# Kernel optimization log

Hardware: AMD Instinct MI355X
Metric: run time of the kernel (lower is better)

## Reference

```python
import jax, jax.numpy as jnp
import numpy as np

T, B, I, H = 512, 256, 256, 256


def setup_inputs() -> dict:
    key = jax.random.key(0)
    ks = jax.random.split(key, 4)
    s = 1.0 / np.sqrt(I + H)  # fan-in scaling like nn.Linear default
    return {
        "x": jax.random.normal(ks[0], (T, B, I), dtype=jnp.float32),
        "h": jnp.zeros((B, H), dtype=jnp.float32),
        "Wz_w": jax.random.normal(ks[1], (H, I + H), dtype=jnp.float32) * s,
        "Wz_b": jnp.zeros((H,), dtype=jnp.float32),
        "Wr_w": jax.random.normal(ks[2], (H, I + H), dtype=jnp.float32) * s,
        "Wr_b": jnp.zeros((H,), dtype=jnp.float32),
        "W_w": jax.random.normal(ks[3], (H, I + H), dtype=jnp.float32) * s,
        "W_b": jnp.zeros((H,), dtype=jnp.float32),
    }


def reference(x, h, Wz_w, Wz_b, Wr_w, Wr_b, W_w, W_b):
    # x: [T, B, I], h: [B, H]. Gate input order is cat(h, x) as in the torch code.
    def step(h, xt):
        gate = jnp.concatenate([h, xt], axis=1)              # [B, H+I]
        zt = jax.nn.sigmoid(gate @ Wz_w.T + Wz_b)            # [B, H]
        rt = jax.nn.sigmoid(gate @ Wr_w.T + Wr_b)            # [B, H]
        cand_in = jnp.concatenate([rt * h, xt], axis=1)      # [B, H+I]
        ht = (1.0 - zt) * h + zt * jnp.tanh(cand_in @ W_w.T + W_b)
        return ht, ht

    h_final, hAll = jax.lax.scan(step, h, x)                 # hAll: [T, B, H]
    return hAll, h_final
```

## Files before the change

### kernel.cpp

```cpp
#include <hip/hip_runtime.h>


typedef float f32x4 __attribute__((ext_vector_type(4)));
typedef short bf16x8 __attribute__((ext_vector_type(8)));

__device__ __forceinline__ unsigned short f2bf(float f) {
  union { float f; unsigned int u; } v; v.f = f;
  unsigned int u = v.u + 0x7fffu + ((v.u >> 16) & 1u);
  return (unsigned short)(u >> 16);
}
__device__ __forceinline__ float u2f(unsigned int u) {
  union { unsigned int u; float f; } v; v.u = u; return v.f;
}
__device__ __forceinline__ unsigned int cvt_pk_bf16(float lo, float hi) {
  unsigned int r;
  asm("v_cvt_pk_bf16_f32 %0, %1, %2" : "=v"(r) : "v"(lo), "v"(hi));
  return r;
}
__device__ __forceinline__ float sigmoid_f(float x) {
  return __builtin_amdgcn_rcpf(1.f + __expf(-x));
}
__device__ __forceinline__ float tanh_f(float x) {
  float e = __expf(2.f * x);
  return 1.f - 2.f * __builtin_amdgcn_rcpf(e + 1.f);
}
__device__ __forceinline__ f32x4 unpk(uint2 gv) {
  f32x4 a;
  a[0] = u2f(gv.x << 16); a[1] = u2f(gv.x & 0xffff0000u);
  a[2] = u2f(gv.y << 16); a[3] = u2f(gv.y & 0xffff0000u);
  return a;
}
__device__ __forceinline__ int frag_off(int j, int b) {
  return ((j >> 5) * 64 + ((j >> 3) & 3) * 16 + b) * 8 + (j & 7);
}

__global__ __launch_bounds__(256) void gru_gx_kernel(
    const float* __restrict__ x,
    const float* __restrict__ Wz, const float* __restrict__ Wr, const float* __restrict__ Wc,
    const float* __restrict__ bz, const float* __restrict__ br, const float* __restrict__ bc,
    unsigned short* __restrict__ gx)
{
  __shared__ __align__(16) unsigned short As[64][72];
  __shared__ __align__(16) unsigned short Bs[64][72];

  const int tid  = threadIdx.x;
  const int lane = tid & 63;
  const int wid  = tid >> 6;
  const int l15  = lane & 15;
  const int lg   = lane >> 4;
  const int m0   = blockIdx.x * 64;
  const int by   = blockIdx.y;
  const int gate = by >> 2;
  const int jb   = (by & 3) * 64;
  const float* W    = (gate == 0) ? Wz : ((gate == 1) ? Wr : Wc);
  const float* bias = (gate == 0) ? bz : ((gate == 1) ? br : bc);

  f32x4 acc[4];
  #pragma unroll
  for (int n = 0; n < 4; ++n) acc[n] = (f32x4){0.f, 0.f, 0.f, 0.f};

  for (int k0 = 0; k0 < 256; k0 += 64) {
    #pragma unroll
    for (int i = 0; i < 4; ++i) {
      int idx = tid + i * 256;
      int row = idx >> 4;
      int kq  = (idx & 15) << 2;
      float4 va = *(const float4*)(x + (size_t)(m0 + row) * 256 + k0 + kq);
      ushort4 ua; ua.x = f2bf(va.x); ua.y = f2bf(va.y); ua.z = f2bf(va.z); ua.w = f2bf(va.w);
      *(ushort4*)&As[row][kq] = ua;
      float4 vb = *(const float4*)(W + (size_t)(jb + row) * 512 + 256 + k0 + kq);
      ushort4 ub; ub.x = f2bf(vb.x); ub.y = f2bf(vb.y); ub.z = f2bf(vb.z); ub.w = f2bf(vb.w);
      *(ushort4*)&Bs[row][kq] = ub;
    }
    __syncthreads();
    #pragma unroll
    for (int ks = 0; ks < 64; ks += 32) {
      bf16x8 af = *(const bf16x8*)&As[wid * 16 + l15][ks + lg * 8];
      #pragma unroll
      for (int n = 0; n < 4; ++n) {
        bf16x8 bf = *(const bf16x8*)&Bs[n * 16 + l15][ks + lg * 8];
        acc[n] = __builtin_amdgcn_mfma_f32_16x16x32_bf16(af, bf, acc[n], 0, 0, 0);
      }
    }
    __syncthreads();
  }

  #pragma unroll
  for (int n = 0; n < 4; ++n) {
    float bv = bias[jb + n * 16 + l15];
    #pragma unroll
    for (int r = 0; r < 4; ++r) {
      As[wid * 16 + lg * 4 + r][n * 16 + l15] = f2bf(acc[n][r] + bv);
    }
  }
  __syncthreads();

  const int tt    = m0 >> 8;
  const int b0    = m0 & 255;
  const int jbase = by * 64;
  #pragma unroll
  for (int i = 0; i < 2; ++i) {
    int u    = tid + i * 256;
    int bg_l = u >> 7;
    int rem  = u & 127;
    int cb_l = rem >> 3;
    int bp   = rem & 7;
    int row0 = bg_l * 16 + bp * 2;
    uint2 lo = *(const uint2*)&As[row0][cb_l * 4];
    uint2 hi = *(const uint2*)&As[row0 + 1][cb_l * 4];
    uint4 val; val.x = lo.x; val.y = lo.y; val.z = hi.x; val.w = hi.y;
    size_t off = (((size_t)tt * 16 + (b0 >> 4) + bg_l) * 192 + (jbase >> 2) + cb_l) * 64
                 + (size_t)bp * 8;
    *(uint4*)(gx + off) = val;
  }
}

__global__ __launch_bounds__(512, 1) void gru_rec_kernel(
    const unsigned short* __restrict__ gx,
    const float* __restrict__ h0,
    const float* __restrict__ Wz, const float* __restrict__ Wr, const float* __restrict__ Wc,
    float* __restrict__ out)
{
  __shared__ __align__(16) unsigned short hA[4096];
  __shared__ __align__(16) unsigned short rhA[4096];

  const int tid   = threadIdx.x;
  const int lane  = tid & 63;
  const int wid   = tid >> 6;
  const int l15   = lane & 15;
  const int lg    = lane >> 4;
  const int wg    = blockIdx.x;
  const int brow0 = wg * 16;
  const int cb    = wid * 32;

  bf16x8 wz[2][8], wr[2][8], wc[2][8];
  #pragma unroll
  for (int n = 0; n < 2; ++n) {
    const int j = cb + n * 16 + l15;
    #pragma unroll
    for (int kk = 0; kk < 8; ++kk) {
      const int k = kk * 32 + lg * 8;
      #pragma unroll
      for (int g = 0; g < 3; ++g) {
        const float* W = (g == 0) ? Wz : ((g == 1) ? Wr : Wc);
        const float* p = W + (size_t)j * 512 + k;
        float4 a = *(const float4*)p;
        float4 b = *(const float4*)(p + 4);
        bf16x8 f;
        f[0] = (short)f2bf(a.x); f[1] = (short)f2bf(a.y);
        f[2] = (short)f2bf(a.z); f[3] = (short)f2bf(a.w);
        f[4] = (short)f2bf(b.x); f[5] = (short)f2bf(b.y);
        f[6] = (short)f2bf(b.z); f[7] = (short)f2bf(b.w);
        if (g == 0) wz[n][kk] = f; else if (g == 1) wr[n][kk] = f; else wc[n][kk] = f;
      }
    }
  }

  f32x4 hreg[2];
  #pragma unroll
  for (int n = 0; n < 2; ++n)
    hreg[n] = *(const f32x4*)(h0 + (size_t)(brow0 + l15) * 256 + cb + n * 16 + lg * 4);
  for (int idx = tid; idx < 16 * 256; idx += 512) {
    int r = idx >> 8, c = idx & 255;
    hA[frag_off(c, r)] = f2bf(h0[(size_t)(brow0 + r) * 256 + c]);
  }

  uint2 g1z[2], g1r[2], g2[2];
  {
    const size_t tb = (size_t)wg * 12288;
    #pragma unroll
    for (int n = 0; n < 2; ++n) {
      g1z[n] = *(const uint2*)(gx + tb + (size_t)(wid * 8 + n * 4 + lg) * 64 + l15 * 4);
      g1r[n] = *(const uint2*)(gx + tb + (size_t)(64 + wid * 8 + n * 4 + lg) * 64 + l15 * 4);
      g2[n]  = *(const uint2*)(gx + tb + (size_t)(128 + wid * 8 + n * 4 + lg) * 64 + l15 * 4);
    }
  }
  __syncthreads();

  for (int t = 0; t < 512; ++t) {
    const int tn = (t < 511) ? (t + 1) : 511;
    const size_t tbn = ((size_t)tn * 16 + wg) * 12288;

    f32x4 accZ[2], accR[2];
    #pragma unroll
    for (int n = 0; n < 2; ++n) { accZ[n] = unpk(g1z[n]); accR[n] = unpk(g1r[n]); }
    #pragma unroll
    for (int n = 0; n < 2; ++n) {
      g1z[n] = *(const uint2*)(gx + tbn + (size_t)(wid * 8 + n * 4 + lg) * 64 + l15 * 4);
      g1r[n] = *(const uint2*)(gx + tbn + (size_t)(64 + wid * 8 + n * 4 + lg) * 64 + l15 * 4);
    }

    #pragma unroll
    for (int kk = 0; kk < 8; ++kk) {
      bf16x8 hf = *(const bf16x8*)&hA[kk * 512 + lane * 8];
      accZ[0] = __builtin_amdgcn_mfma_f32_16x16x32_bf16(wz[0][kk], hf, accZ[0], 0, 0, 0);
      accZ[1] = __builtin_amdgcn_mfma_f32_16x16x32_bf16(wz[1][kk], hf, accZ[1], 0, 0, 0);
      accR[0] = __builtin_amdgcn_mfma_f32_16x16x32_bf16(wr[0][kk], hf, accR[0], 0, 0, 0);
      accR[1] = __builtin_amdgcn_mfma_f32_16x16x32_bf16(wr[1][kk], hf, accR[1], 0, 0, 0);
    }
    f32x4 zreg[2];
    #pragma unroll
    for (int n = 0; n < 2; ++n) {
      #pragma unroll
      for (int r = 0; r < 4; ++r) zreg[n][r] = sigmoid_f(accZ[n][r]);
      float rh0 = sigmoid_f(accR[n][0]) * hreg[n][0];
      float rh1 = sigmoid_f(accR[n][1]) * hreg[n][1];
      float rh2 = sigmoid_f(accR[n][2]) * hreg[n][2];
      float rh3 = sigmoid_f(accR[n][3]) * hreg[n][3];
      uint2 pk; pk.x = cvt_pk_bf16(rh0, rh1); pk.y = cvt_pk_bf16(rh2, rh3);
      *(uint2*)&rhA[frag_off(cb + n * 16 + lg * 4, l15)] = pk;
    }
    asm volatile("s_waitcnt lgkmcnt(0)" ::: "memory");
    __builtin_amdgcn_s_barrier();
    __builtin_amdgcn_sched_barrier(0);

    f32x4 acc2[2];
    #pragma unroll
    for (int n = 0; n < 2; ++n) acc2[n] = unpk(g2[n]);
    #pragma unroll
    for (int n = 0; n < 2; ++n)
      g2[n] = *(const uint2*)(gx + tbn + (size_t)(128 + wid * 8 + n * 4 + lg) * 64 + l15 * 4);

    #pragma unroll
    for (int kk = 0; kk < 8; ++kk) {
      bf16x8 rf = *(const bf16x8*)&rhA[kk * 512 + lane * 8];
      acc2[0] = __builtin_amdgcn_mfma_f32_16x16x32_bf16(wc[0][kk], rf, acc2[0], 0, 0, 0);
      acc2[1] = __builtin_amdgcn_mfma_f32_16x16x32_bf16(wc[1][kk], rf, acc2[1], 0, 0, 0);
    }
    #pragma unroll
    for (int n = 0; n < 2; ++n) {
      #pragma unroll
      for (int r = 0; r < 4; ++r) {
        float th = tanh_f(acc2[n][r]);
        hreg[n][r] = hreg[n][r] + zreg[n][r] * (th - hreg[n][r]);
      }
      *(f32x4*)(out + (size_t)t * 65536 + (size_t)(brow0 + l15) * 256 + cb + n * 16 + lg * 4) = hreg[n];
      if (t == 511)
        *(f32x4*)(out + (size_t)33554432 + (size_t)(brow0 + l15) * 256 + cb + n * 16 + lg * 4) = hreg[n];
      uint2 pk; pk.x = cvt_pk_bf16(hreg[n][0], hreg[n][1]);
      pk.y = cvt_pk_bf16(hreg[n][2], hreg[n][3]);
      *(uint2*)&hA[frag_off(cb + n * 16 + lg * 4, l15)] = pk;
    }
    asm volatile("s_waitcnt lgkmcnt(0)" ::: "memory");
    __builtin_amdgcn_s_barrier();
    __builtin_amdgcn_sched_barrier(0);
  }
}

extern "C" void kernel_launch(void* const* d_in, const int* in_sizes, int n_in,
                              void* d_out, int out_size, void* d_ws, size_t ws_size,
                              hipStream_t stream) {
  const float* x  = (const float*)d_in[0];
  const float* h0 = (const float*)d_in[1];
  const float* Wz = (const float*)d_in[2];
  const float* bz = (const float*)d_in[3];
  const float* Wr = (const float*)d_in[4];
  const float* br = (const float*)d_in[5];
  const float* Wc = (const float*)d_in[6];
  const float* bc = (const float*)d_in[7];
  float* out = (float*)d_out;
  unsigned short* gxbuf = (unsigned short*)d_ws;

  dim3 gridA(2048, 12);
  gru_gx_kernel<<<gridA, 256, 0, stream>>>(x, Wz, Wr, Wc, bz, br, bc, gxbuf);
  gru_rec_kernel<<<16, 512, 0, stream>>>(gxbuf, h0, Wz, Wr, Wc, out);
}
```

Before: 1.146 ms.

## Widen input-projection tile to full gate width to reuse x loads

The input-projection GEMM kernel now computes all 256 output columns of a gate per block instead of 64. Each x tile is loaded and converted once per gate rather than four times, and the grid shrinks from 12 to 3 blocks in y. Conversion to bf16 now uses the packed v_cvt_pk_bf16 instruction. In exchange each block holds 16 accumulators, uses a 36KB B tile in LDS, and still re-reads the weights in every block, which raises register and LDS pressure and lowers occupancy.

```diff
diff --git a/kernel.cpp b/kernel.cpp
--- a/kernel.cpp
+++ b/kernel.cpp
@@ -41,7 +41,7 @@
     unsigned short* __restrict__ gx)
 {
   __shared__ __align__(16) unsigned short As[64][72];
-  __shared__ __align__(16) unsigned short Bs[64][72];
+  __shared__ __align__(16) unsigned short Bs[256][72];
 
   const int tid  = threadIdx.x;
   const int lane = tid & 63;
@@ -49,15 +49,13 @@
   const int l15  = lane & 15;
   const int lg   = lane >> 4;
   const int m0   = blockIdx.x * 64;
-  const int by   = blockIdx.y;
-  const int gate = by >> 2;
-  const int jb   = (by & 3) * 64;
+  const int gate = blockIdx.y;
   const float* W    = (gate == 0) ? Wz : ((gate == 1) ? Wr : Wc);
   const float* bias = (gate == 0) ? bz : ((gate == 1) ? br : bc);
 
-  f32x4 acc[4];
-  #pragma unroll
-  for (int n = 0; n < 4; ++n) acc[n] = (f32x4){0.f, 0.f, 0.f, 0.f};
+  f32x4 acc[16];
+  #pragma unroll
+  for (int n = 0; n < 16; ++n) acc[n] = (f32x4){0.f, 0.f, 0.f, 0.f};
 
   for (int k0 = 0; k0 < 256; k0 += 64) {
     #pragma unroll
@@ -65,19 +63,25 @@
       int idx = tid + i * 256;
       int row = idx >> 4;
       int kq  = (idx & 15) << 2;
-      float4 va = *(const float4*)(x + (size_t)(m0 + row) * 256 + k0 + kq);
-      ushort4 ua; ua.x = f2bf(va.x); ua.y = f2bf(va.y); ua.z = f2bf(va.z); ua.w = f2bf(va.w);
-      *(ushort4*)&As[row][kq] = ua;
-      float4 vb = *(const float4*)(W + (size_t)(jb + row) * 512 + 256 + k0 + kq);
-      ushort4 ub; ub.x = f2bf(vb.x); ub.y = f2bf(vb.y); ub.z = f2bf(vb.z); ub.w = f2bf(vb.w);
-      *(ushort4*)&Bs[row][kq] = ub;
+      float4 v = *(const float4*)(x + (size_t)(m0 + row) * 256 + k0 + kq);
+      uint2 p; p.x = cvt_pk_bf16(v.x, v.y); p.y = cvt_pk_bf16(v.z, v.w);
+      *(uint2*)&As[row][kq] = p;
+    }
+    #pragma unroll
+    for (int i = 0; i < 16; ++i) {
+      int idx = tid + i * 256;
+      int row = idx >> 4;
+      int kq  = (idx & 15) << 2;
+      float4 v = *(const float4*)(W + (size_t)row * 512 + 256 + k0 + kq);
+      uint2 p; p.x = cvt_pk_bf16(v.x, v.y); p.y = cvt_pk_bf16(v.z, v.w);
+      *(uint2*)&Bs[row][kq] = p;
     }
     __syncthreads();
     #pragma unroll
     for (int ks = 0; ks < 64; ks += 32) {
       bf16x8 af = *(const bf16x8*)&As[wid * 16 + l15][ks + lg * 8];
       #pragma unroll
-      for (int n = 0; n < 4; ++n) {
+      for (int n = 0; n < 16; ++n) {
         bf16x8 bf = *(const bf16x8*)&Bs[n * 16 + l15][ks + lg * 8];
         acc[n] = __builtin_amdgcn_mfma_f32_16x16x32_bf16(af, bf, acc[n], 0, 0, 0);
       }
@@ -85,31 +89,34 @@
     __syncthreads();
   }
 
-  #pragma unroll
-  for (int n = 0; n < 4; ++n) {
-    float bv = bias[jb + n * 16 + l15];
+  unsigned short* Ts = &Bs[0][0];
+  const int TS = 268;
+  #pragma unroll
+  for (int n = 0; n < 16; ++n) {
+    const int j = n * 16 + l15;
+    float bv = bias[j];
     #pragma unroll
     for (int r = 0; r < 4; ++r) {
-      As[wid * 16 + lg * 4 + r][n * 16 + l15] = f2bf(acc[n][r] + bv);
+      unsigned int pk = cvt_pk_bf16(acc[n][r] + bv, 0.f);
+      Ts[(wid * 16 + lg * 4 + r) * TS + j] = (unsigned short)pk;
     }
   }
   __syncthreads();
 
-  const int tt    = m0 >> 8;
-  const int b0    = m0 & 255;
-  const int jbase = by * 64;
-  #pragma unroll
-  for (int i = 0; i < 2; ++i) {
-    int u    = tid + i * 256;
-    int bg_l = u >> 7;
-    int rem  = u & 127;
+  const int tt  = m0 >> 8;
+  const int bg0 = (m0 & 255) >> 4;
+  #pragma unroll
+  for (int i = 0; i < 8; ++i) {
+    int idx  = tid + i * 256;
+    int bg_l = idx >> 9;
+    int rem  = idx & 511;
     int cb_l = rem >> 3;
     int bp   = rem & 7;
-    int row0 = bg_l * 16 + bp * 2;
-    uint2 lo = *(const uint2*)&As[row0][cb_l * 4];
-    uint2 hi = *(const uint2*)&As[row0 + 1][cb_l * 4];
+    int m    = bg_l * 16 + bp * 2;
+    uint2 lo = *(const uint2*)&Ts[(size_t)m * TS + cb_l * 4];
+    uint2 hi = *(const uint2*)&Ts[(size_t)(m + 1) * TS + cb_l * 4];
     uint4 val; val.x = lo.x; val.y = lo.y; val.z = hi.x; val.w = hi.y;
-    size_t off = (((size_t)tt * 16 + (b0 >> 4) + bg_l) * 192 + (jbase >> 2) + cb_l) * 64
+    size_t off = (((size_t)tt * 16 + bg0 + bg_l) * 192 + gate * 64 + cb_l) * 64
                  + (size_t)bp * 8;
     *(uint4*)(gx + off) = val;
   }
@@ -261,7 +268,7 @@
   float* out = (float*)d_out;
   unsigned short* gxbuf = (unsigned short*)d_ws;
 
-  dim3 gridA(2048, 12);
+  dim3 gridA(2048, 3);
   gru_gx_kernel<<<gridA, 256, 0, stream>>>(x, Wz, Wr, Wc, bz, br, bc, gxbuf);
   gru_rec_kernel<<<16, 512, 0, stream>>>(gxbuf, h0, Wz, Wr, Wc, out);
 }
```

Measured after the change: 1.042 ms, median of 3. -9.1%, faster.
